# Kernel optimization log

Hardware: AMD Instinct MI355X
Metric: run time of the kernel (lower is better)

## Reference

```python
import jax, jax.numpy as jnp
import numpy as np

V = 50000      # word vocab
CV = 63        # char vocab (60 chars + 3 tags)
HW = 512       # word hidden size
HC = 256       # char hidden size
NLW = 2        # word lstm layers
NLC = 2        # char lstm layers
L = 12         # chars in the word


def _lstm_layers(x, H, C, Wih, Whh, bih, bhh):
    """One time-step of a multi-layer LSTM (PyTorch gate order i,f,g,o).
    x: [1, D], H/C: [nl, 1, D]. Returns (top_h, newH, newC)."""
    nl = Wih.shape[0]
    newH, newC = [], []
    inp = x
    for l in range(nl):
        gates = inp @ Wih[l].T + H[l] @ Whh[l].T + bih[l] + bhh[l]  # [1, 4D]
        i, f, g, o = jnp.split(gates, 4, axis=-1)
        i = jax.nn.sigmoid(i)
        f = jax.nn.sigmoid(f)
        g = jnp.tanh(g)
        o = jax.nn.sigmoid(o)
        c = f * C[l] + i * g
        h = o * jnp.tanh(c)
        newH.append(h)
        newC.append(c)
        inp = h
    return inp, jnp.stack(newH), jnp.stack(newC)


def setup_inputs() -> dict:
    key = jax.random.key(0)
    ks = jax.random.split(key, 20)
    sW = 1.0 / np.sqrt(HW)
    sC = 1.0 / np.sqrt(HC)
    return {
        "x_word": jax.random.randint(ks[0], (1,), 0, V),
        "x_char": jax.random.randint(ks[1], (L,), 0, CV),
        "h_word_h": jax.random.normal(ks[2], (NLW, 1, HW), jnp.float32),
        "h_word_c": jax.random.normal(ks[3], (NLW, 1, HW), jnp.float32),
        "h_char_h": jax.random.normal(ks[4], (NLC, 1, HC), jnp.float32),
        "h_char_c": jax.random.normal(ks[5], (NLC, 1, HC), jnp.float32),
        "word_emb": jax.random.normal(ks[6], (V, HW), jnp.float32),
        "word_Wih": jax.random.normal(ks[7], (NLW, 4 * HW, HW), jnp.float32) * sW,
        "word_Whh": jax.random.normal(ks[8], (NLW, 4 * HW, HW), jnp.float32) * sW,
        "word_bih": jax.random.normal(ks[9], (NLW, 4 * HW), jnp.float32) * sW,
        "word_bhh": jax.random.normal(ks[10], (NLW, 4 * HW), jnp.float32) * sW,
        "dec_W": jax.random.normal(ks[11], (V, HW), jnp.float32) * sW,
        "dec_b": jax.random.normal(ks[12], (V,), jnp.float32) * sW,
        "char_emb": jax.random.normal(ks[13], (CV, HC), jnp.float32),
        "char_Wih": jax.random.normal(ks[14], (NLC, 4 * HC, HC), jnp.float32) * sC,
        "char_Whh": jax.random.normal(ks[15], (NLC, 4 * HC, HC), jnp.float32) * sC,
        "char_bih": jax.random.normal(ks[16], (NLC, 4 * HC), jnp.float32) * sC,
        "char_bhh": jax.random.normal(ks[17], (NLC, 4 * HC), jnp.float32) * sC,
        "char_to_embedding": jax.random.normal(ks[18], (HW, HC), jnp.float32),
        "g_w": jax.random.normal(ks[19], (HW,), jnp.float32) * sW,
        "g_b": jax.random.normal(jax.random.fold_in(key, 99), (1,), jnp.float32),
    }


def reference(x_word, x_char, h_word_h, h_word_c, h_char_h, h_char_c,
              word_emb, word_Wih, word_Whh, word_bih, word_bhh,
              dec_W, dec_b,
              char_emb, char_Wih, char_Whh, char_bih, char_bhh,
              char_to_embedding, g_w, g_b):
    # character-level recurrence over the word's characters
    def char_step(carry, cidx):
        H, C = carry
        xc = char_emb[cidx][None, :]  # [1, HC]
        _, H, C = _lstm_layers(xc, H, C, char_Wih, char_Whh, char_bih, char_bhh)
        return (H, C), None

    (h_char_h, h_char_c), _ = jax.lax.scan(char_step, (h_char_h, h_char_c), x_char)

    # note: original uses h_char[1] (the CELL state) of the last layer
    x_c = char_to_embedding @ h_char_c[-1].T          # [HW, 1]
    x_w = word_emb[x_word[0]][None, :]                # [1, HW]
    g = jax.nn.relu(jnp.dot(g_w, x_w[0]) + g_b[0])    # scalar gate
    x = (1.0 - g) * x_w + g * x_c.T                   # [1, HW]

    y, h_word_h, h_word_c = _lstm_layers(x, h_word_h, h_word_c,
                                         word_Wih, word_Whh, word_bih, word_bhh)
    y = y @ dec_W.T + dec_b                           # [1, V]
    return y, h_word_h, h_word_c, h_char_h, h_char_c
```

## Files before the change

### kernel.cpp

```cpp
#include <hip/hip_runtime.h>
#include <stdint.h>


#define SCOPE_AGT __HIP_MEMORY_SCOPE_AGENT
#define ALL64 0xFFFFFFFFFFFFFFFFull

static __device__ __forceinline__ float dot4(float4 w, const float* p){
    return w.x*p[0] + w.y*p[1] + w.z*p[2] + w.w*p[3];
}
static __device__ __forceinline__ float dot44(float4 a, float4 b){
    return a.x*b.x + a.y*b.y + a.z*b.z + a.w*b.w;
}
static __device__ __forceinline__ float sigf(float x){ return 1.0f / (1.0f + __expf(-x)); }
static __device__ __forceinline__ float tanhf_(float x){
    x = fminf(fmaxf(x, -15.0f), 15.0f);
    float e = __expf(2.0f * x);
    return (e - 1.0f) / (e + 1.0f);
}

static __device__ __forceinline__ float gload(const float* p){
    return __hip_atomic_load(p, __ATOMIC_RELAXED, SCOPE_AGT);
}
static __device__ __forceinline__ void gstore(float* p, float v){
    __hip_atomic_store(p, v, __ATOMIC_RELAXED, SCOPE_AGT);
}
static __device__ __forceinline__ int gload_i(const int* p){
    return __hip_atomic_load(p, __ATOMIC_RELAXED, SCOPE_AGT);
}
static __device__ __forceinline__ void gstore_i(int* p, int v){
    __hip_atomic_store(p, v, __ATOMIC_RELAXED, SCOPE_AGT);
}
static __device__ __forceinline__ unsigned long long gload_ll(const float* p){
    return __hip_atomic_load((const unsigned long long*)p, __ATOMIC_RELAXED, SCOPE_AGT);
}
static __device__ __forceinline__ void gstore_ll(float* p, unsigned long long v){
    __hip_atomic_store((unsigned long long*)p, v, __ATOMIC_RELAXED, SCOPE_AGT);
}

union PairU { unsigned long long u; float f[2]; };

__global__ __launch_bounds__(256, 2) void k_fused(
    const int* __restrict__ x_word, const int* __restrict__ x_char,
    const float* __restrict__ hwh, const float* __restrict__ hwc,
    const float* __restrict__ hch, const float* __restrict__ hcc,
    const float* __restrict__ word_emb,
    const float* __restrict__ wWih, const float* __restrict__ wWhh,
    const float* __restrict__ wbih, const float* __restrict__ wbhh,
    const float* __restrict__ dec_W, const float* __restrict__ dec_b,
    const float* __restrict__ char_emb,
    const float* __restrict__ cWih, const float* __restrict__ cWhh,
    const float* __restrict__ cbih, const float* __restrict__ cbhh,
    const float* __restrict__ cte,
    const float* __restrict__ g_w, const float* __restrict__ g_b,
    float* __restrict__ ws, float* __restrict__ out)
{
    const int tid  = threadIdx.x;
    const int bx   = blockIdx.x;
    const int lane = tid & 63;
    const int wv   = tid >> 6;
    int*   ws_i  = (int*)(ws + 4096);
    int*   w0f   = ws_i;
    int*   w1f   = ws_i + 128;
    int*   cdone = ws_i + 256;
    float* fdata = ws + 6400;

    __shared__ float sHW[512];

    if (bx < 64){
        __shared__ float sH1[256], sH2[256], sE[256], sg1[16], sg2[16];

        const int rg = tid >> 4, lane16 = tid & 15;
        const int gate = rg & 3, uu = rg >> 2;
        const int u = (bx << 2) + uu;
        const int row = (gate << 8) + u, row2 = 1024 + row;

        float4 w1i[4], w1h[4], w2i[4], w2h[4];
        {
            const float4* p1i = (const float4*)(cWih + (size_t)row  * 256) + lane16 * 4;
            const float4* p1h = (const float4*)(cWhh + (size_t)row  * 256) + lane16 * 4;
            const float4* p2i = (const float4*)(cWih + (size_t)row2 * 256) + lane16 * 4;
            const float4* p2h = (const float4*)(cWhh + (size_t)row2 * 256) + lane16 * 4;
            #pragma unroll
            for (int j = 0; j < 4; ++j){ w1i[j]=p1i[j]; w1h[j]=p1h[j]; w2i[j]=p2i[j]; w2h[j]=p2h[j]; }
        }
        const float b1 = cbih[row]  + cbhh[row];
        const float b2 = cbih[row2] + cbhh[row2];

        float c1r = 0.f, c2r = 0.f, h1fin = 0.f, h2fin = 0.f;
        if (tid < 4)      c1r = hcc[(bx<<2) + tid];
        else if (tid < 8) c2r = hcc[256 + (bx<<2) + (tid-4)];

        for (int t = 0; t <= 12; ++t){
            if (t == 0){
                sH1[tid] = hch[tid];
            } else {
                if (t == 1) sH2[tid] = hch[256 + tid];
                if (tid < 64){
                    const int p = (t - 1) & 1;
                    const float* base = fdata + (size_t)(p*64 + tid)*32;
                    const float ft = (float)t;
                    if (t >= 2){
                        while (true){
                            PairU q[8];
                            #pragma unroll
                            for (int k = 0; k < 8; ++k) q[k].u = gload_ll(base + 2*k);
                            bool ok = true;
                            #pragma unroll
                            for (int k = 0; k < 8; ++k) ok &= (q[k].f[1] == ft);
                            if (__ballot(ok) == ALL64){
                                #pragma unroll
                                for (int k = 0; k < 4; ++k){
                                    sH1[4*tid + k] = q[k].f[0];
                                    sH2[4*tid + k] = q[4+k].f[0];
                                }
                                break;
                            }
                        }
                    } else {
                        while (true){
                            PairU q[4];
                            #pragma unroll
                            for (int k = 0; k < 4; ++k) q[k].u = gload_ll(base + 2*k);
                            bool ok = true;
                            #pragma unroll
                            for (int k = 0; k < 4; ++k) ok &= (q[k].f[1] == ft);
                            if (__ballot(ok) == ALL64){
                                #pragma unroll
                                for (int k = 0; k < 4; ++k) sH1[4*tid + k] = q[k].f[0];
                                break;
                            }
                        }
                    }
                }
            }
            if (t < 12) sE[tid] = char_emb[x_char[t]*256 + tid];
            __syncthreads();

            float a1 = 0.f, a2 = 0.f;
            if (t < 12){
                const float* xp = sE  + lane16*16;
                const float* hp = sH1 + lane16*16;
                #pragma unroll
                for (int j = 0; j < 4; ++j) a1 += dot4(w1i[j], xp + 4*j) + dot4(w1h[j], hp + 4*j);
            }
            if (t >= 1){
                const float* xp = sH1 + lane16*16;
                const float* hp = sH2 + lane16*16;
                #pragma unroll
                for (int j = 0; j < 4; ++j) a2 += dot4(w2i[j], xp + 4*j) + dot4(w2h[j], hp + 4*j);
            }
            #pragma unroll
            for (int m = 8; m >= 1; m >>= 1){
                a1 += __shfl_xor(a1, m, 64);
                a2 += __shfl_xor(a2, m, 64);
            }
            if (lane16 == 0){
                if (t < 12) sg1[rg] = a1 + b1;
                if (t >= 1) sg2[rg] = a2 + b2;
            }
            __syncthreads();

            float* dst = fdata + (size_t)((t & 1)*64 + bx)*32;
            if (tid < 4){
                if (t < 12){
                    float gi = sigf(sg1[tid*4+0]);
                    float gf = sigf(sg1[tid*4+1]);
                    float gg = tanhf_(sg1[tid*4+2]);
                    float go = sigf(sg1[tid*4+3]);
                    float c = gf * c1r + gi * gg;
                    c1r = c;
                    float h = go * tanhf_(c);
                    h1fin = h;
                    PairU pr; pr.f[0] = h; pr.f[1] = (float)(t+1);
                    gstore_ll(dst + 2*tid, pr.u);
                }
            } else if (tid < 8){
                if (t >= 1){
                    int q = tid - 4;
                    float gi = sigf(sg2[q*4+0]);
                    float gf = sigf(sg2[q*4+1]);
                    float gg = tanhf_(sg2[q*4+2]);
                    float go = sigf(sg2[q*4+3]);
                    float c = gf * c2r + gi * gg;
                    c2r = c;
                    float h = go * tanhf_(c);
                    h2fin = h;
                    PairU pr; pr.f[0] = (t < 12) ? h : c;
                    pr.f[1] = (float)(t+1);
                    gstore_ll(dst + 8 + 2*q, pr.u);
                }
            }
            __syncthreads();
        }

        if (tid < 4){
            int uh = (bx << 2) + tid;
            out[52048 + uh] = h1fin;
            out[52560 + uh] = c1r;
        } else if (tid < 8){
            int uh = (bx << 2) + (tid - 4);
            out[52048 + 256 + uh] = h2fin;
            out[52560 + 256 + uh] = c2r;
        }

        if (bx == 0 && tid < 64){
            const float* base = fdata + (size_t)tid*32;
            while (true){
                PairU q[4];
                #pragma unroll
                for (int k = 0; k < 4; ++k) q[k].u = gload_ll(base + 8 + 2*k);
                bool ok = true;
                #pragma unroll
                for (int k = 0; k < 4; ++k) ok &= (q[k].f[1] == 13.0f);
                if (__ballot(ok) == ALL64) break;
            }
            gstore_i(cdone + tid*32, 1);
        }

    } else if (bx < 192){
        __shared__ float sC2[256];
        __shared__ float sXCW[512];
        __shared__ float sMisc[8];
        const int vw = ((bx - 64) << 2) + wv;
        float4 wi0[4], wi1[4], wh0[4], wh1[4]; float bs[4];
        #pragma unroll
        for (int gq = 0; gq < 4; ++gq){
            const size_t rf = (size_t)((gq << 9) + vw);
            const float4* pi = (const float4*)(wWih + rf*512) + lane*2;
            const float4* ph = (const float4*)(wWhh + rf*512) + lane*2;
            wi0[gq] = pi[0]; wi1[gq] = pi[1];
            wh0[gq] = ph[0]; wh1[gq] = ph[1];
            bs[gq] = wbih[rf] + wbhh[rf];
        }
        const float4* hv = (const float4*)(hwh) + lane*2;
        const float4 hva = hv[0], hvb = hv[1];
        const size_t wbase = (size_t)x_word[0] * 512;
        const float4* wep = (const float4*)(word_emb + wbase) + lane*2;
        const float4 wea = wep[0], web = wep[1];

        if (bx == 64){
            float p = g_w[2*tid]   * word_emb[wbase + 2*tid]
                    + g_w[2*tid+1] * word_emb[wbase + 2*tid+1];
            #pragma unroll
            for (int m = 32; m >= 1; m >>= 1) p += __shfl_xor(p, m, 64);
            if (lane == 0) sMisc[wv] = p;
            __syncthreads();
            if (tid == 0)
                gstore(ws + 3072, fmaxf(sMisc[0]+sMisc[1]+sMisc[2]+sMisc[3] + g_b[0], 0.0f));
        }

        if (tid == 0){
            int* myline = cdone + ((bx - 64) & 63)*32;
            while (gload_i(myline) < 1) __builtin_amdgcn_s_sleep(4);
        }
        __syncthreads();
        {
            PairU q;
            q.u = gload_ll(fdata + (size_t)(tid >> 2)*32 + 8 + 2*(tid & 3));
            sC2[tid] = q.f[0];
        }
        __syncthreads();

        {
            float4 cv  = ((const float4*)(cte + (size_t)vw*256))[lane];
            float4 c2v = ((const float4*)sC2)[lane];
            float acc = dot44(cv, c2v);
            #pragma unroll
            for (int m = 32; m >= 1; m >>= 1) acc += __shfl_xor(acc, m, 64);
            if (lane == 0) gstore(ws + 1536 + vw, acc);
        }
        __syncthreads();
        if (tid == 0) gstore_i(w0f + (bx - 64), 1);
        if (tid < 64){
            while (true){
                unsigned long long v = gload_ll((const float*)(w0f + 2*tid));
                int lo = (int)(v & 0xffffffffu), hi = (int)(v >> 32);
                if (__ballot(lo >= 1 && hi >= 1) == ALL64) break;
            }
        }
        __syncthreads();
        sXCW[tid]       = gload(ws + 1536 + tid);
        sXCW[256 + tid] = gload(ws + 1536 + 256 + tid);
        if (tid == 0) sMisc[4] = gload(ws + 3072);
        __syncthreads();

        {
            const float g  = sMisc[4];
            const float og = 1.0f - g;
            const float4 x0 = ((const float4*)sXCW)[lane*2];
            const float4 x1 = ((const float4*)sXCW)[lane*2 + 1];
            float4 xa, xb;
            xa.x = og*wea.x + g*x0.x; xa.y = og*wea.y + g*x0.y;
            xa.z = og*wea.z + g*x0.z; xa.w = og*wea.w + g*x0.w;
            xb.x = og*web.x + g*x1.x; xb.y = og*web.y + g*x1.y;
            xb.z = og*web.z + g*x1.z; xb.w = og*web.w + g*x1.w;
            float ac[4];
            #pragma unroll
            for (int gq = 0; gq < 4; ++gq){
                float a = dot44(wi0[gq], xa) + dot44(wi1[gq], xb)
                        + dot44(wh0[gq], hva) + dot44(wh1[gq], hvb);
                #pragma unroll
                for (int m = 32; m >= 1; m >>= 1) a += __shfl_xor(a, m, 64);
                ac[gq] = a;
            }
            if (lane == 0){
                float gi = sigf(ac[0] + bs[0]);
                float gf = sigf(ac[1] + bs[1]);
                float gg = tanhf_(ac[2] + bs[2]);
                float go = sigf(ac[3] + bs[3]);
                float c = gf * hwc[vw] + gi * gg;
                float h = go * tanhf_(c);
                gstore(ws + 2048 + vw, h);
                out[50000 + vw] = h;
                out[51024 + vw] = c;
            }
        }
        __syncthreads();
        if (tid == 0) gstore_i(w0f + (bx - 64), 2);

    } else {
        __shared__ float sX1[512];
        const int vw = ((bx - 192) << 2) + wv;
        float4 wi0[4], wi1[4], wh0[4], wh1[4]; float bs[4];
        #pragma unroll
        for (int gq = 0; gq < 4; ++gq){
            const size_t rf = (size_t)(2048 + (gq << 9) + vw);
            const float4* pi = (const float4*)(wWih + rf*512) + lane*2;
            const float4* ph = (const float4*)(wWhh + rf*512) + lane*2;
            wi0[gq] = pi[0]; wi1[gq] = pi[1];
            wh0[gq] = ph[0]; wh1[gq] = ph[1];
            bs[gq] = wbih[rf] + wbhh[rf];
        }
        const float4* hv = (const float4*)(hwh + 512) + lane*2;
        const float4 hva = hv[0], hvb = hv[1];

        if (tid < 64){
            while (true){
                unsigned long long v = gload_ll((const float*)(w0f + 2*tid));
                int lo = (int)(v & 0xffffffffu), hi = (int)(v >> 32);
                if (__ballot(lo >= 2 && hi >= 2) == ALL64) break;
                __builtin_amdgcn_s_sleep(2);
            }
        }
        __syncthreads();
        sX1[tid]       = gload(ws + 2048 + tid);
        sX1[256 + tid] = gload(ws + 2048 + 256 + tid);
        __syncthreads();
        {
            const float4 xa = ((const float4*)sX1)[lane*2];
            const float4 xb = ((const float4*)sX1)[lane*2 + 1];
            float ac[4];
            #pragma unroll
            for (int gq = 0; gq < 4; ++gq){
                float a = dot44(wi0[gq], xa) + dot44(wi1[gq], xb)
                        + dot44(wh0[gq], hva) + dot44(wh1[gq], hvb);
                #pragma unroll
                for (int m = 32; m >= 1; m >>= 1) a += __shfl_xor(a, m, 64);
                ac[gq] = a;
            }
            if (lane == 0){
                float gi = sigf(ac[0] + bs[0]);
                float gf = sigf(ac[1] + bs[1]);
                float gg = tanhf_(ac[2] + bs[2]);
                float go = sigf(ac[3] + bs[3]);
                float c = gf * hwc[512 + vw] + gi * gg;
                float h = go * tanhf_(c);
                gstore(ws + 2560 + vw, h);
                out[50000 + 512 + vw] = h;
                out[51024 + 512 + vw] = c;
            }
        }
        __syncthreads();
        if (tid == 0) gstore_i(w1f + (bx - 192), 1);
    }

    if (tid < 64){
        while (true){
            unsigned long long v = gload_ll((const float*)(w1f + 2*tid));
            int lo = (int)(v & 0xffffffffu), hi = (int)(v >> 32);
            if (__ballot(lo >= 1 && hi >= 1) == ALL64) break;
            __builtin_amdgcn_s_sleep(8);
        }
    }
    __syncthreads();
    sHW[tid]       = gload(ws + 2560 + tid);
    sHW[256 + tid] = gload(ws + 2560 + 256 + tid);
    __syncthreads();
    {
        const int wid  = (bx << 2) + wv;
        const int cc   = lane & 31;
        const int half = lane >> 5;
        float4 hq[4];
        const float4* sf4 = (const float4*)sHW;
        #pragma unroll
        for (int j = 0; j < 4; ++j) hq[j] = sf4[cc + j*32];

        for (int r0 = wid*2; r0 < 50000; r0 += 2560){
            const int r = r0 + half;
            const float4* wp = (const float4*)(dec_W + (size_t)r*512) + cc;
            float4 wb[4];
            #pragma unroll
            for (int j = 0; j < 4; ++j) wb[j] = wp[j*32];
            float acc = 0.f;
            #pragma unroll
            for (int j = 0; j < 4; ++j) acc += dot44(wb[j], hq[j]);
            acc += __shfl_xor(acc, 1, 64);
            acc += __shfl_xor(acc, 2, 64);
            acc += __shfl_xor(acc, 4, 64);
            acc += __shfl_xor(acc, 8, 64);
            acc += __shfl_xor(acc, 16, 64);
            if (cc == 0) out[r] = acc + dec_b[r];
        }
    }
}

extern "C" void kernel_launch(void* const* d_in, const int* in_sizes, int n_in,
                              void* d_out, int out_size, void* d_ws, size_t ws_size,
                              hipStream_t stream)
{
    const int*   x_word   = (const int*)d_in[0];
    const int*   x_char   = (const int*)d_in[1];
    const float* hwh      = (const float*)d_in[2];
    const float* hwc      = (const float*)d_in[3];
    const float* hch      = (const float*)d_in[4];
    const float* hcc      = (const float*)d_in[5];
    const float* word_emb = (const float*)d_in[6];
    const float* wWih     = (const float*)d_in[7];
    const float* wWhh     = (const float*)d_in[8];
    const float* wbih     = (const float*)d_in[9];
    const float* wbhh     = (const float*)d_in[10];
    const float* dec_W    = (const float*)d_in[11];
    const float* dec_b    = (const float*)d_in[12];
    const float* char_emb = (const float*)d_in[13];
    const float* cWih     = (const float*)d_in[14];
    const float* cWhh     = (const float*)d_in[15];
    const float* cbih     = (const float*)d_in[16];
    const float* cbhh     = (const float*)d_in[17];
    const float* cte      = (const float*)d_in[18];
    const float* g_w      = (const float*)d_in[19];
    const float* g_b      = (const float*)d_in[20];

    float* ws  = (float*)d_ws;
    float* out = (float*)d_out;

    hipMemsetAsync((void*)((char*)d_ws + 16384), 0, 32768, stream);

    hipLaunchKernelGGL(k_fused, dim3(320), dim3(256), 0, stream,
        x_word, x_char, hwh, hwc, hch, hcc, word_emb,
        wWih, wWhh, wbih, wbhh, dec_W, dec_b,
        char_emb, cWih, cWhh, cbih, cbhh, cte, g_w, g_b,
        ws, out);
}
```

Baseline: 299.4 us.

## Replace flag-based inter-block sync with replicated value+tag mailboxes

Drops the separate done-flag arrays used for cross-block handoff. Each stage now publishes its values paired with a validity tag into several replicated mailbox copies, and consumers poll the data directly using wide cache-bypassing loads (sc0 sc1 inline asm). The goal is to remove a flag round-trip and spread polling traffic across replicas. All 12 char embeddings are also preloaded into LDS up front, and the memset is widened to cover the new workspace regions, at the cost of more LDS use and extra stores for the replicas.

Result: faster. 287.0 us (-4.1%).

```diff
diff --git a/kernel.cpp b/kernel.cpp
--- a/kernel.cpp
+++ b/kernel.cpp
@@ -18,26 +18,43 @@
     return (e - 1.0f) / (e + 1.0f);
 }
 
-static __device__ __forceinline__ float gload(const float* p){
-    return __hip_atomic_load(p, __ATOMIC_RELAXED, SCOPE_AGT);
-}
-static __device__ __forceinline__ void gstore(float* p, float v){
-    __hip_atomic_store(p, v, __ATOMIC_RELAXED, SCOPE_AGT);
-}
-static __device__ __forceinline__ int gload_i(const int* p){
-    return __hip_atomic_load(p, __ATOMIC_RELAXED, SCOPE_AGT);
-}
-static __device__ __forceinline__ void gstore_i(int* p, int v){
-    __hip_atomic_store(p, v, __ATOMIC_RELAXED, SCOPE_AGT);
+static __device__ __forceinline__ void gstore_ll(float* p, unsigned long long v){
+    __hip_atomic_store((unsigned long long*)p, v, __ATOMIC_RELAXED, SCOPE_AGT);
 }
 static __device__ __forceinline__ unsigned long long gload_ll(const float* p){
     return __hip_atomic_load((const unsigned long long*)p, __ATOMIC_RELAXED, SCOPE_AGT);
 }
-static __device__ __forceinline__ void gstore_ll(float* p, unsigned long long v){
-    __hip_atomic_store((unsigned long long*)p, v, __ATOMIC_RELAXED, SCOPE_AGT);
-}
 
 union PairU { unsigned long long u; float f[2]; };
+
+static __device__ __forceinline__ float4 sc_load16(const float* p){
+    float4 r;
+    asm volatile("global_load_dwordx4 %0, %1, off sc0 sc1\n\t"
+                 "s_waitcnt vmcnt(0)"
+                 : "=&v"(r) : "v"(p) : "memory");
+    return r;
+}
+static __device__ __forceinline__ void sc_load32(const float* p, float4& a, float4& b){
+    asm volatile("global_load_dwordx4 %0, %2, off sc0 sc1\n\t"
+                 "global_load_dwordx4 %1, %2, off offset:16 sc0 sc1\n\t"
+                 "s_waitcnt vmcnt(0)"
+                 : "=&v"(a), "=&v"(b) : "v"(p) : "memory");
+}
+static __device__ __forceinline__ void sc_load64(const float* p, float4& a, float4& b,
+                                                 float4& c, float4& d){
+    asm volatile("global_load_dwordx4 %0, %4, off sc0 sc1\n\t"
+                 "global_load_dwordx4 %1, %4, off offset:16 sc0 sc1\n\t"
+                 "global_load_dwordx4 %2, %4, off offset:32 sc0 sc1\n\t"
+                 "global_load_dwordx4 %3, %4, off offset:48 sc0 sc1\n\t"
+                 "s_waitcnt vmcnt(0)"
+                 : "=&v"(a), "=&v"(b), "=&v"(c), "=&v"(d) : "v"(p) : "memory");
+}
+
+#define WS_C2   8192
+#define WS_XCW  9216
+#define WS_HW1  11264
+#define WS_HW2  13312
+#define WS_G    17408
 
 __global__ __launch_bounds__(256, 2) void k_fused(
     const int* __restrict__ x_word, const int* __restrict__ x_char,
@@ -58,16 +75,13 @@
     const int bx   = blockIdx.x;
     const int lane = tid & 63;
     const int wv   = tid >> 6;
-    int*   ws_i  = (int*)(ws + 4096);
-    int*   w0f   = ws_i;
-    int*   w1f   = ws_i + 128;
-    int*   cdone = ws_i + 256;
-    float* fdata = ws + 6400;
 
     __shared__ float sHW[512];
 
     if (bx < 64){
-        __shared__ float sH1[256], sH2[256], sE[256], sg1[16], sg2[16];
+        __shared__ float sH1[256], sH2[256], sg1[16], sg2[16], sPub[8];
+        __shared__ float sEall[12][256];
+        __shared__ int   sXC[12];
 
         const int rg = tid >> 4, lane16 = tid & 15;
         const int gate = rg & 3, uu = rg >> 2;
@@ -85,6 +99,10 @@
         }
         const float b1 = cbih[row]  + cbhh[row];
         const float b2 = cbih[row2] + cbhh[row2];
+
+        if (tid < 12) sXC[tid] = x_char[tid];
+        __syncthreads();
+        for (int s = 0; s < 12; ++s) sEall[s][tid] = char_emb[sXC[s]*256 + tid];
 
         float c1r = 0.f, c2r = 0.f, h1fin = 0.f, h2fin = 0.f;
         if (tid < 4)      c1r = hcc[(bx<<2) + tid];
@@ -97,48 +115,38 @@
                 if (t == 1) sH2[tid] = hch[256 + tid];
                 if (tid < 64){
                     const int p = (t - 1) & 1;
-                    const float* base = fdata + (size_t)(p*64 + tid)*32;
+                    const float* base = ws + ((size_t)((p*64 + tid)*4 + (bx & 3)) * 16);
                     const float ft = (float)t;
                     if (t >= 2){
                         while (true){
-                            PairU q[8];
-                            #pragma unroll
-                            for (int k = 0; k < 8; ++k) q[k].u = gload_ll(base + 2*k);
-                            bool ok = true;
-                            #pragma unroll
-                            for (int k = 0; k < 8; ++k) ok &= (q[k].f[1] == ft);
+                            float4 a,b,c,d;
+                            sc_load64(base, a, b, c, d);
+                            bool ok = (a.y==ft)&&(a.w==ft)&&(b.y==ft)&&(b.w==ft)
+                                   && (c.y==ft)&&(c.w==ft)&&(d.y==ft)&&(d.w==ft);
                             if (__ballot(ok) == ALL64){
-                                #pragma unroll
-                                for (int k = 0; k < 4; ++k){
-                                    sH1[4*tid + k] = q[k].f[0];
-                                    sH2[4*tid + k] = q[4+k].f[0];
-                                }
+                                sH1[4*tid+0]=a.x; sH1[4*tid+1]=a.z; sH1[4*tid+2]=b.x; sH1[4*tid+3]=b.z;
+                                sH2[4*tid+0]=c.x; sH2[4*tid+1]=c.z; sH2[4*tid+2]=d.x; sH2[4*tid+3]=d.z;
                                 break;
                             }
                         }
                     } else {
                         while (true){
-                            PairU q[4];
-                            #pragma unroll
-                            for (int k = 0; k < 4; ++k) q[k].u = gload_ll(base + 2*k);
-                            bool ok = true;
-                            #pragma unroll
-                            for (int k = 0; k < 4; ++k) ok &= (q[k].f[1] == ft);
+                            float4 a,b;
+                            sc_load32(base, a, b);
+                            bool ok = (a.y==ft)&&(a.w==ft)&&(b.y==ft)&&(b.w==ft);
                             if (__ballot(ok) == ALL64){
-                                #pragma unroll
-                                for (int k = 0; k < 4; ++k) sH1[4*tid + k] = q[k].f[0];
+                                sH1[4*tid+0]=a.x; sH1[4*tid+1]=a.z; sH1[4*tid+2]=b.x; sH1[4*tid+3]=b.z;
                                 break;
                             }
                         }
                     }
                 }
             }
-            if (t < 12) sE[tid] = char_emb[x_char[t]*256 + tid];
             __syncthreads();
 
             float a1 = 0.f, a2 = 0.f;
             if (t < 12){
-                const float* xp = sE  + lane16*16;
+                const float* xp = &sEall[t][0] + lane16*16;
                 const float* hp = sH1 + lane16*16;
                 #pragma unroll
                 for (int j = 0; j < 4; ++j) a1 += dot4(w1i[j], xp + 4*j) + dot4(w1h[j], hp + 4*j);
@@ -160,7 +168,6 @@
             }
             __syncthreads();
 
-            float* dst = fdata + (size_t)((t & 1)*64 + bx)*32;
             if (tid < 4){
                 if (t < 12){
                     float gi = sigf(sg1[tid*4+0]);
@@ -171,8 +178,7 @@
                     c1r = c;
                     float h = go * tanhf_(c);
                     h1fin = h;
-                    PairU pr; pr.f[0] = h; pr.f[1] = (float)(t+1);
-                    gstore_ll(dst + 2*tid, pr.u);
+                    sPub[tid] = h;
                 }
             } else if (tid < 8){
                 if (t >= 1){
@@ -185,12 +191,27 @@
                     c2r = c;
                     float h = go * tanhf_(c);
                     h2fin = h;
-                    PairU pr; pr.f[0] = (t < 12) ? h : c;
-                    pr.f[1] = (float)(t+1);
-                    gstore_ll(dst + 8 + 2*q, pr.u);
+                    sPub[tid] = (t < 12) ? h : c;
                 }
             }
             __syncthreads();
+
+            if (t < 12){
+                if (tid < 32){
+                    const int rep = tid >> 3, k = tid & 7;
+                    const bool valid = (k < 4) ? true : (t >= 1);
+                    if (valid){
+                        PairU pr; pr.f[0] = sPub[k]; pr.f[1] = (float)(t+1);
+                        gstore_ll(ws + ((size_t)(((t&1)*64 + bx)*4 + rep) * 16) + 2*k, pr.u);
+                    }
+                }
+            } else {
+                if (tid < 8){
+                    const int rep = tid >> 2, uq = tid & 3;
+                    PairU pr; pr.f[0] = sPub[4+uq]; pr.f[1] = 13.0f;
+                    gstore_ll(ws + WS_C2 + rep*512 + ((bx<<2)+uq)*2, pr.u);
+                }
+            }
         }
 
         if (tid < 4){
@@ -203,25 +224,11 @@
             out[52560 + 256 + uh] = c2r;
         }
 
-        if (bx == 0 && tid < 64){
-            const float* base = fdata + (size_t)tid*32;
-            while (true){
-                PairU q[4];
-                #pragma unroll
-                for (int k = 0; k < 4; ++k) q[k].u = gload_ll(base + 8 + 2*k);
-                bool ok = true;
-                #pragma unroll
-                for (int k = 0; k < 4; ++k) ok &= (q[k].f[1] == 13.0f);
-                if (__ballot(ok) == ALL64) break;
-            }
-            gstore_i(cdone + tid*32, 1);
-        }
-
     } else if (bx < 192){
-        __shared__ float sC2[256];
-        __shared__ float sXCW[512];
-        __shared__ float sMisc[8];
-        const int vw = ((bx - 64) << 2) + wv;
+        __shared__ float sC2[256], sXCW[512], sAcc[8], sG[4], sH0[4];
+        const int mb = bx - 64;
+        const int vwb = mb << 2;
+        const int vw = vwb + wv;
         float4 wi0[4], wi1[4], wh0[4], wh1[4]; float bs[4];
         #pragma unroll
         for (int gq = 0; gq < 4; ++gq){
@@ -243,21 +250,32 @@
                     + g_w[2*tid+1] * word_emb[wbase + 2*tid+1];
             #pragma unroll
             for (int m = 32; m >= 1; m >>= 1) p += __shfl_xor(p, m, 64);
-            if (lane == 0) sMisc[wv] = p;
+            if (lane == 0) sAcc[wv] = p;
             __syncthreads();
-            if (tid == 0)
-                gstore(ws + 3072, fmaxf(sMisc[0]+sMisc[1]+sMisc[2]+sMisc[3] + g_b[0], 0.0f));
+            if (tid == 0){
+                float gg = fmaxf(sAcc[0]+sAcc[1]+sAcc[2]+sAcc[3] + g_b[0], 0.0f);
+                PairU pr; pr.f[0] = gg; pr.f[1] = 1.0f;
+                gstore_ll(ws + WS_G, pr.u);
+                gstore_ll(ws + WS_G + 32, pr.u);
+            }
+            __syncthreads();
         }
 
         if (tid == 0){
-            int* myline = cdone + ((bx - 64) & 63)*32;
-            while (gload_i(myline) < 1) __builtin_amdgcn_s_sleep(4);
-        }
-        __syncthreads();
-        {
-            PairU q;
-            q.u = gload_ll(fdata + (size_t)(tid >> 2)*32 + 8 + 2*(tid & 3));
-            sC2[tid] = q.f[0];
+            const float* sp = ws + WS_C2 + (bx & 1)*512 + ((bx*37) & 255)*2;
+            while (true){
+                PairU q; q.u = gload_ll(sp);
+                if (q.f[1] == 13.0f) break;
+                __builtin_amdgcn_s_sleep(2);
+            }
+        }
+        __syncthreads();
+        {
+            const float* cb = ws + WS_C2 + (bx & 1)*512;
+            while (true){
+                PairU q; q.u = gload_ll(cb + tid*2);
+                if (__ballot(q.f[1] == 13.0f) == ALL64){ sC2[tid] = q.f[0]; break; }
+            }
         }
         __syncthreads();
 
@@ -267,25 +285,33 @@
             float acc = dot44(cv, c2v);
             #pragma unroll
             for (int m = 32; m >= 1; m >>= 1) acc += __shfl_xor(acc, m, 64);
-            if (lane == 0) gstore(ws + 1536 + vw, acc);
-        }
-        __syncthreads();
-        if (tid == 0) gstore_i(w0f + (bx - 64), 1);
-        if (tid < 64){
+            if (lane == 0) sAcc[wv] = acc;
+        }
+        __syncthreads();
+        if (tid < 8){
+            const int rep = tid >> 2, uq = tid & 3;
+            PairU pr; pr.f[0] = sAcc[uq]; pr.f[1] = 1.0f;
+            gstore_ll(ws + WS_XCW + rep*1024 + (vwb+uq)*2, pr.u);
+        }
+        if (tid == 1){
             while (true){
-                unsigned long long v = gload_ll((const float*)(w0f + 2*tid));
-                int lo = (int)(v & 0xffffffffu), hi = (int)(v >> 32);
-                if (__ballot(lo >= 1 && hi >= 1) == ALL64) break;
-            }
-        }
-        __syncthreads();
-        sXCW[tid]       = gload(ws + 1536 + tid);
-        sXCW[256 + tid] = gload(ws + 1536 + 256 + tid);
-        if (tid == 0) sMisc[4] = gload(ws + 3072);
-        __syncthreads();
-
-        {
-            const float g  = sMisc[4];
+                PairU q; q.u = gload_ll(ws + WS_G + (bx & 1)*32);
+                if (q.f[1] == 1.0f){ sG[0] = q.f[0]; break; }
+            }
+        }
+        {
+            const float* xb = ws + WS_XCW + (bx & 1)*1024;
+            while (true){
+                float4 v4 = sc_load16(xb + 4*tid);
+                if (__ballot(v4.y == 1.0f && v4.w == 1.0f) == ALL64){
+                    sXCW[2*tid] = v4.x; sXCW[2*tid+1] = v4.z; break;
+                }
+            }
+        }
+        __syncthreads();
+
+        {
+            const float g  = sG[0];
             const float og = 1.0f - g;
             const float4 x0 = ((const float4*)sXCW)[lane*2];
             const float4 x1 = ((const float4*)sXCW)[lane*2 + 1];
@@ -310,17 +336,23 @@
                 float go = sigf(ac[3] + bs[3]);
                 float c = gf * hwc[vw] + gi * gg;
                 float h = go * tanhf_(c);
-                gstore(ws + 2048 + vw, h);
+                sH0[wv] = h;
                 out[50000 + vw] = h;
                 out[51024 + vw] = c;
             }
         }
         __syncthreads();
-        if (tid == 0) gstore_i(w0f + (bx - 64), 2);
+        if (tid < 8){
+            const int rep = tid >> 2, uq = tid & 3;
+            PairU pr; pr.f[0] = sH0[uq]; pr.f[1] = 1.0f;
+            gstore_ll(ws + WS_HW1 + rep*1024 + (vwb+uq)*2, pr.u);
+        }
 
     } else {
-        __shared__ float sX1[512];
-        const int vw = ((bx - 192) << 2) + wv;
+        __shared__ float sX1[512], sH1v[4];
+        const int mb = bx - 192;
+        const int vwb = mb << 2;
+        const int vw = vwb + wv;
         float4 wi0[4], wi1[4], wh0[4], wh1[4]; float bs[4];
         #pragma unroll
         for (int gq = 0; gq < 4; ++gq){
@@ -334,17 +366,24 @@
         const float4* hv = (const float4*)(hwh + 512) + lane*2;
         const float4 hva = hv[0], hvb = hv[1];
 
-        if (tid < 64){
+        if (tid == 0){
+            const float* sp = ws + WS_HW1 + (bx & 1)*1024 + ((bx*37) & 511)*2;
             while (true){
-                unsigned long long v = gload_ll((const float*)(w0f + 2*tid));
-                int lo = (int)(v & 0xffffffffu), hi = (int)(v >> 32);
-                if (__ballot(lo >= 2 && hi >= 2) == ALL64) break;
-                __builtin_amdgcn_s_sleep(2);
-            }
-        }
-        __syncthreads();
-        sX1[tid]       = gload(ws + 2048 + tid);
-        sX1[256 + tid] = gload(ws + 2048 + 256 + tid);
+                PairU q; q.u = gload_ll(sp);
+                if (q.f[1] == 1.0f) break;
+                __builtin_amdgcn_s_sleep(4);
+            }
+        }
+        __syncthreads();
+        {
+            const float* xb = ws + WS_HW1 + (bx & 1)*1024;
+            while (true){
+                float4 v4 = sc_load16(xb + 4*tid);
+                if (__ballot(v4.y == 1.0f && v4.w == 1.0f) == ALL64){
+                    sX1[2*tid] = v4.x; sX1[2*tid+1] = v4.z; break;
+                }
+            }
+        }
         __syncthreads();
         {
             const float4 xa = ((const float4*)sX1)[lane*2];
@@ -365,26 +404,37 @@
                 float go = sigf(ac[3] + bs[3]);
                 float c = gf * hwc[512 + vw] + gi * gg;
                 float h = go * tanhf_(c);
-                gstore(ws + 2560 + vw, h);
+                sH1v[wv] = h;
                 out[50000 + 512 + vw] = h;
                 out[51024 + 512 + vw] = c;
             }
         }
         __syncthreads();
-        if (tid == 0) gstore_i(w1f + (bx - 192), 1);
+        if (tid < 16){
+            const int rep = tid >> 2, uq = tid & 3;
+            PairU pr; pr.f[0] = sH1v[uq]; pr.f[1] = 1.0f;
+            gstore_ll(ws + WS_HW2 + rep*1024 + (vwb+uq)*2, pr.u);
+        }
     }
 
-    if (tid < 64){
+    if (tid == 0){
+        const float* sp = ws + WS_HW2 + (bx & 3)*1024 + ((bx*37) & 511)*2;
         while (true){
-            unsigned long long v = gload_ll((const float*)(w1f + 2*tid));
-            int lo = (int)(v & 0xffffffffu), hi = (int)(v >> 32);
-            if (__ballot(lo >= 1 && hi >= 1) == ALL64) break;
-            __builtin_amdgcn_s_sleep(8);
+            PairU q; q.u = gload_ll(sp);
+            if (q.f[1] == 1.0f) break;
+            __builtin_amdgcn_s_sleep(4);
         }
     }
     __syncthreads();
-    sHW[tid]       = gload(ws + 2560 + tid);
-    sHW[256 + tid] = gload(ws + 2560 + 256 + tid);
+    {
+        const float* hb = ws + WS_HW2 + (bx & 3)*1024;
+        while (true){
+            float4 v4 = sc_load16(hb + 4*tid);
+            if (__ballot(v4.y == 1.0f && v4.w == 1.0f) == ALL64){
+                sHW[2*tid] = v4.x; sHW[2*tid+1] = v4.z; break;
+            }
+        }
+    }
     __syncthreads();
     {
         const int wid  = (bx << 2) + wv;
@@ -443,7 +493,7 @@
     float* ws  = (float*)d_ws;
     float* out = (float*)d_out;
 
-    hipMemsetAsync((void*)((char*)d_ws + 16384), 0, 32768, stream);
+    hipMemsetAsync(d_ws, 0, 69888, stream);
 
     hipLaunchKernelGGL(k_fused, dim3(320), dim3(256), 0, stream,
         x_word, x_char, hwh, hwc, hch, hcc, word_emb,
```
